# Optimization experiments

Measured on AMD Instinct MI355X. Metric: run time of the kernel, lower is better.

The kernel has to match this reference:

```python
import jax, jax.numpy as jnp
import numpy as np

D_MODEL = 4096
N_HEADS = 32
N_KV_HEADS = 8
HEAD_DIM = D_MODEL // N_HEADS  # 128
SEQ = 2048
BATCH = 1
ROPE_BASE = 10000.0


def build_rope_cache(max_seq_len, head_dim, base=10000.0):
    half = head_dim // 2
    pos = jnp.arange(max_seq_len, dtype=jnp.float32)
    inv_freqs = 1.0 / (base ** (jnp.arange(half, dtype=jnp.float32) / half))
    angles = pos[:, None] * inv_freqs[None, :]  # (S, half)
    return jnp.cos(angles), jnp.sin(angles)


def apply_rope(t, cos, sin):
    # t: (B, H, S, D); cos/sin: (S, D//2) broadcast over batch & heads.
    t_even = t[..., 0::2]
    t_odd = t[..., 1::2]
    c = cos[None, None, :, :]
    s = sin[None, None, :, :]
    rot_even = t_even * c - t_odd * s
    rot_odd = t_even * s + t_odd * c
    # interleave back into even/odd slots
    return jnp.stack([rot_even, rot_odd], axis=-1).reshape(t.shape)


def setup_inputs() -> dict:
    key = jax.random.key(0)
    kx, kq, kk, kv, ko = jax.random.split(key, 5)
    bound = 1.0 / np.sqrt(D_MODEL)
    x = jax.random.normal(kx, (BATCH, SEQ, D_MODEL), dtype=jnp.float32)
    # torch Linear weights: (out_features, in_features)
    wq = jax.random.uniform(kq, (N_HEADS * HEAD_DIM, D_MODEL), minval=-bound, maxval=bound, dtype=jnp.float32)
    wk = jax.random.uniform(kk, (N_KV_HEADS * HEAD_DIM, D_MODEL), minval=-bound, maxval=bound, dtype=jnp.float32)
    wv = jax.random.uniform(kv, (N_KV_HEADS * HEAD_DIM, D_MODEL), minval=-bound, maxval=bound, dtype=jnp.float32)
    wo = jax.random.uniform(ko, (D_MODEL, D_MODEL), minval=-bound, maxval=bound, dtype=jnp.float32)
    attn_mask = jnp.tril(jnp.ones((SEQ, SEQ), dtype=jnp.int32))[None, None, :, :]
    return {"x": x, "wq": wq, "wk": wk, "wv": wv, "wo": wo, "attn_mask": attn_mask}


def reference(x, wq, wk, wv, wo, attn_mask):
    B, S, _ = x.shape
    cos, sin = build_rope_cache(SEQ, HEAD_DIM, ROPE_BASE)
    cos, sin = cos[:S], sin[:S]
    q = (x @ wq.T).reshape(B, S, N_HEADS, HEAD_DIM).transpose(0, 2, 1, 3)      # (B,H,S,D)
    k = (x @ wk.T).reshape(B, S, N_KV_HEADS, HEAD_DIM).transpose(0, 2, 1, 3)   # (B,Hkv,S,D)
    v = (x @ wv.T).reshape(B, S, N_KV_HEADS, HEAD_DIM).transpose(0, 2, 1, 3)
    q = apply_rope(q, cos, sin)
    k = apply_rope(k, cos, sin)
    n_rep = N_HEADS // N_KV_HEADS
    if n_rep > 1:
        k = jnp.repeat(k, n_rep, axis=1)
        v = jnp.repeat(v, n_rep, axis=1)
    scores = jnp.einsum('bhqd,bhkd->bhqk', q, k) / jnp.sqrt(jnp.float32(HEAD_DIM))
    scores = jnp.where(attn_mask == 0, -jnp.inf, scores)
    attn = jax.nn.softmax(scores, axis=-1)
    out = jnp.einsum('bhqk,bhkd->bhqd', attn, v)
    out = out.transpose(0, 2, 1, 3).reshape(B, S, D_MODEL)
    return out @ wo.T
```

## Files before the change

### kernel.cpp

```cpp
#include <hip/hip_runtime.h>
#include <hip/hip_bf16.h>

typedef float f32x2 __attribute__((ext_vector_type(2)));
typedef float f32x4 __attribute__((ext_vector_type(4)));
typedef __bf16 bf16x4 __attribute__((ext_vector_type(4)));
typedef __bf16 bf16x8 __attribute__((ext_vector_type(8)));

__device__ __forceinline__ void gld_lds16(const void* g, void* l) {
  __builtin_amdgcn_global_load_lds((const __attribute__((address_space(1))) void*)g,
                                   (__attribute__((address_space(3))) void*)l, 16, 0, 0);
}

__global__ void cvt_f32_bf16(const float* __restrict__ in, __bf16* __restrict__ out,
                             int n8) {
  int idx = blockIdx.x * blockDim.x + threadIdx.x;
  if (idx >= n8) return;
  f32x4 a = *(const f32x4*)(in + (size_t)idx * 8);
  f32x4 b = *(const f32x4*)(in + (size_t)idx * 8 + 4);
  bf16x8 o;
#pragma unroll
  for (int j = 0; j < 4; ++j) { o[j] = (__bf16)a[j]; o[4 + j] = (__bf16)b[j]; }
  *(bf16x8*)(out + (size_t)idx * 8) = o;
}

__global__ void cvt_f32_bf16_2(const float* __restrict__ inA,
                               const float* __restrict__ inB,
                               __bf16* __restrict__ out, int n8half) {
  int idx = blockIdx.x * blockDim.x + threadIdx.x;
  if (idx >= 2 * n8half) return;
  const float* src = (idx < n8half) ? inA + (size_t)idx * 8
                                    : inB + (size_t)(idx - n8half) * 8;
  f32x4 a = *(const f32x4*)src;
  f32x4 b = *(const f32x4*)(src + 4);
  bf16x8 o;
#pragma unroll
  for (int j = 0; j < 4; ++j) { o[j] = (__bf16)a[j]; o[4 + j] = (__bf16)b[j]; }
  *(bf16x8*)(out + (size_t)idx * 8) = o;
}

__global__ void cvt_x_trig(const float* __restrict__ in, __bf16* __restrict__ out,
                           int n8, float* __restrict__ trig, int ntrig) {
  int idx = blockIdx.x * blockDim.x + threadIdx.x;
  if (idx < n8) {
    f32x4 a = *(const f32x4*)(in + (size_t)idx * 8);
    f32x4 b = *(const f32x4*)(in + (size_t)idx * 8 + 4);
    bf16x8 o;
#pragma unroll
    for (int j = 0; j < 4; ++j) { o[j] = (__bf16)a[j]; o[4 + j] = (__bf16)b[j]; }
    *(bf16x8*)(out + (size_t)idx * 8) = o;
  } else if (idx - n8 < ntrig) {
    int t = idx - n8;
    int i = t & 63, s = t >> 6;
    float ang = (float)s * powf(10000.0f, -(float)i * (1.0f / 64.0f));
    float sn, cs;
    sincosf(ang, &sn, &cs);
    trig[t * 2] = cs;
    trig[t * 2 + 1] = sn;
  }
}

template <int BM, int BN, typename OutT, bool KVF>
__global__ __launch_bounds__(256) void gemm_bf16(const __bf16* __restrict__ A,
                                                 const __bf16* __restrict__ B0,
                                                 const __bf16* __restrict__ B1,
                                                 int Nsplit, OutT* __restrict__ C,
                                                 int M, int N, int K,
                                                 const float* __restrict__ trig,
                                                 __bf16* __restrict__ Vt) {
  constexpr int MI = BM / 32, NJ = BN / 32;
  constexpr int RA = BM / 32, RB = BN / 32;
  __shared__ __bf16 As[BM * 64] __attribute__((aligned(16)));
  __shared__ __bf16 Bs[BN * 64] __attribute__((aligned(16)));

  const int tid = threadIdx.x;
  const int lane = tid & 63;
  const int w = tid >> 6;
  const int nwg = gridDim.x * gridDim.y;
  const int orig = blockIdx.y * gridDim.x + blockIdx.x;
  const int wgid = (orig & 7) * (nwg >> 3) + (orig >> 3);
  const int m0 = (wgid % gridDim.x) * BM;
  const int n0 = (wgid / gridDim.x) * BN;
  const int li = lane & 15, lg = lane >> 4;

  const __bf16* bsrc[RB];
#pragma unroll
  for (int i = 0; i < RB; ++i) {
    int slot = i * 256 + w * 64 + lane;
    int row = slot >> 3;
    int sch = (slot & 7) ^ (row & 7);
    int n = n0 + row;
    bsrc[i] = (n < Nsplit ? B0 + (size_t)n * K : B1 + (size_t)(n - Nsplit) * K) +
              sch * 8;
  }
  const __bf16* asrc[RA];
#pragma unroll
  for (int i = 0; i < RA; ++i) {
    int slot = i * 256 + w * 64 + lane;
    int row = slot >> 3;
    int sch = (slot & 7) ^ (row & 7);
    asrc[i] = A + (size_t)(m0 + row) * K + sch * 8;
  }

  const int wr = (w >> 1) * (BM / 2);
  const int wc = (w & 1) * (BN / 2);

  f32x4 acc[MI][NJ] = {};

  for (int k0 = 0; k0 < K; k0 += 64) {
    __syncthreads();
#pragma unroll
    for (int i = 0; i < RA; ++i)
      gld_lds16(asrc[i] + k0, &As[(i * 256 + w * 64) * 8]);
#pragma unroll
    for (int i = 0; i < RB; ++i)
      gld_lds16(bsrc[i] + k0, &Bs[(i * 256 + w * 64) * 8]);
    __syncthreads();

#pragma unroll
    for (int u = 0; u < 2; ++u) {
      bf16x8 af[MI], bfr[NJ];
#pragma unroll
      for (int mi = 0; mi < MI; ++mi)
        af[mi] = *(const bf16x8*)&As[(wr + mi * 16 + li) * 64 +
                                     (((u * 4 + lg) ^ (li & 7)) * 8)];
#pragma unroll
      for (int nj = 0; nj < NJ; ++nj)
        bfr[nj] = *(const bf16x8*)&Bs[(wc + nj * 16 + li) * 64 +
                                      (((u * 4 + lg) ^ (li & 7)) * 8)];
#pragma unroll
      for (int mi = 0; mi < MI; ++mi)
#pragma unroll
        for (int nj = 0; nj < NJ; ++nj)
          acc[mi][nj] = __builtin_amdgcn_mfma_f32_16x16x32_bf16(af[mi], bfr[nj],
                                                                acc[mi][nj], 0, 0, 0);
    }
  }

  const int crow = lg * 4;
  if (KVF && n0 >= Nsplit) {
#pragma unroll
    for (int mi = 0; mi < MI; ++mi)
#pragma unroll
      for (int nj = 0; nj < NJ; ++nj) {
        int d = n0 - Nsplit + wc + nj * 16 + li;
        int sb = m0 + wr + mi * 16 + crow;
        bf16x4 pk;
#pragma unroll
        for (int r = 0; r < 4; ++r) pk[r] = (__bf16)acc[mi][nj][r];
        *(bf16x4*)&Vt[(size_t)d * 2048 + sb] = pk;
      }
  } else if (KVF) {
#pragma unroll
    for (int mi = 0; mi < MI; ++mi)
#pragma unroll
      for (int nj = 0; nj < NJ; ++nj) {
        int c = n0 + wc + nj * 16 + li;
        int i = (c & 127) >> 1;
        bool even = (c & 1) == 0;
#pragma unroll
        for (int r = 0; r < 4; ++r) {
          int s = m0 + wr + mi * 16 + crow + r;
          float own = acc[mi][nj][r];
          float oth = __shfl_xor(own, 1);
          f32x2 cs = *(const f32x2*)&trig[((size_t)s * 64 + i) * 2];
          float v = even ? (own * cs[0] - oth * cs[1])
                         : (oth * cs[1] + own * cs[0]);
          C[(size_t)s * N + c] = (OutT)v;
        }
      }
  } else {
#pragma unroll
    for (int mi = 0; mi < MI; ++mi)
#pragma unroll
      for (int nj = 0; nj < NJ; ++nj)
#pragma unroll
        for (int r = 0; r < 4; ++r)
          C[(size_t)(m0 + wr + mi * 16 + crow + r) * N + (n0 + wc + nj * 16 + li)] =
              (OutT)acc[mi][nj][r];
  }
}

__global__ __launch_bounds__(256) void attn_fwd_v11(const __bf16* __restrict__ Q,
                                                    const __bf16* __restrict__ KVb,
                                                    const __bf16* __restrict__ Vt,
                                                    const float* __restrict__ trig,
                                                    __bf16* __restrict__ O,
                                                    const float* __restrict__ wo,
                                                    __bf16* __restrict__ wob) {
  const int tid = threadIdx.x;
  const int lane = tid & 63;
  const int w = tid >> 6;
  const int bid = blockIdx.x;
  const int xcd = bid & 7;
  const int r9 = bid >> 3;
  const int h = xcd * 4 + (r9 & 3);
  const int mb = 31 - (r9 >> 2);
  const int kvh = h >> 2;
  const int m0 = mb * 64;
  const int rbase = m0 + w * 16;

  __shared__ __bf16 Ks[3][32 * 128] __attribute__((aligned(16)));
  __shared__ __bf16 Vs[3][128 * 32] __attribute__((aligned(16)));
  __shared__ __bf16 Ps[4][16 * 40] __attribute__((aligned(16)));

  const int li = lane & 15, lg = lane >> 4;
  const float qscale = 0.08838834764831845f * 1.4426950408889634f;

  auto stage_k = [&](int k0, int buf) {
#pragma unroll
    for (int i = 0; i < 2; ++i) {
      int slot = i * 256 + tid;
      int row = slot >> 4;
      int sch = (slot & 15) ^ (row & 7);
      gld_lds16(&KVb[(size_t)(k0 + row) * 2048 + kvh * 128 + sch * 8],
                &Ks[buf][(i * 256 + w * 64) * 8]);
    }
  };
  auto stage_v = [&](int k0, int buf) {
#pragma unroll
    for (int i = 0; i < 2; ++i) {
      int slot = i * 256 + tid;
      int row = slot >> 2;
      int sch = (slot & 3) ^ ((row >> 1) & 3);
      gld_lds16(&Vt[(size_t)(kvh * 128 + row) * 2048 + k0 + sch * 8],
                &Vs[buf][(i * 256 + w * 64) * 8]);
    }
  };

  const int s = rbase + li;
  bf16x8 qf[4];
  {
    const __bf16* qrow = Q + (size_t)s * 4096 + h * 128;
#pragma unroll
    for (int kc = 0; kc < 4; ++kc) {
      bf16x8 raw = *(const bf16x8*)(qrow + kc * 32 + lg * 8);
#pragma unroll
      for (int jj = 0; jj < 4; ++jj) {
        int i = kc * 16 + lg * 4 + jj;
        f32x2 cs = *(const f32x2*)&trig[((size_t)s * 64 + i) * 2];
        float e = (float)raw[2 * jj], o = (float)raw[2 * jj + 1];
        qf[kc][2 * jj]     = (__bf16)((e * cs[0] - o * cs[1]) * qscale);
        qf[kc][2 * jj + 1] = (__bf16)((e * cs[1] + o * cs[0]) * qscale);
      }
    }
  }

  f32x4 accO[8] = {};
  float pl[4] = {0.f, 0.f, 0.f, 0.f};
  const int ntile = 2 * (mb + 1);

  stage_v(0, 0);
  stage_k(0, 0);

#pragma unroll 1
  for (int t = 0; t < ntile; ++t) {
    const int k0 = t * 32;
    const int cb = t % 3;
    const int nk = (t + 1 < ntile) ? k0 + 32 : k0;
    stage_v(nk, (t + 1) % 3);
    stage_k(nk, (t + 1) % 3);

    asm volatile("s_waitcnt vmcnt(4)" ::: "memory");
    __builtin_amdgcn_s_barrier();
    __builtin_amdgcn_sched_barrier(0);

    f32x4 s2[2] = {};
    __builtin_amdgcn_s_setprio(1);
#pragma unroll
    for (int nt = 0; nt < 2; ++nt)
#pragma unroll
      for (int kc = 0; kc < 4; ++kc) {
        bf16x8 kf = *(const bf16x8*)&Ks[cb][(li + 16 * nt) * 128 +
                                           (((4 * kc + lg) ^ (li & 7)) * 8)];
        s2[nt] = __builtin_amdgcn_mfma_f32_16x16x32_bf16(kf, qf[kc], s2[nt], 0, 0, 0);
      }
    __builtin_amdgcn_s_setprio(0);

    if (k0 + 31 > rbase) {
#pragma unroll
      for (int nt = 0; nt < 2; ++nt) {
        bf16x4 pk;
#pragma unroll
        for (int rr = 0; rr < 4; ++rr) {
          const int key = k0 + 16 * nt + lg * 4 + rr;
          float v = s2[nt][rr];
          if (key > s) v = -INFINITY;
          float p = exp2f(v);
          pl[rr] += p;
          pk[rr] = (__bf16)p;
        }
        *(bf16x4*)&Ps[w][li * 40 + 16 * nt + lg * 4] = pk;
      }
    } else {
#pragma unroll
      for (int nt = 0; nt < 2; ++nt) {
        bf16x4 pk;
#pragma unroll
        for (int rr = 0; rr < 4; ++rr) {
          float p = exp2f(s2[nt][rr]);
          pl[rr] += p;
          pk[rr] = (__bf16)p;
        }
        *(bf16x4*)&Ps[w][li * 40 + 16 * nt + lg * 4] = pk;
      }
    }
    bf16x8 pa = *(const bf16x8*)&Ps[w][li * 40 + lg * 8];

    __builtin_amdgcn_s_setprio(1);
#pragma unroll
    for (int dt = 0; dt < 8; ++dt) {
      bf16x8 vf = *(const bf16x8*)&Vs[cb][(li + 16 * dt) * 32 +
                                          ((lg ^ ((li >> 1) & 3)) * 8)];
      accO[dt] = __builtin_amdgcn_mfma_f32_16x16x32_bf16(pa, vf, accO[dt], 0, 0, 0);
    }
    __builtin_amdgcn_s_setprio(0);
  }

  {
    float sum = (pl[0] + pl[1]) + (pl[2] + pl[3]);
    sum += __shfl_xor(sum, 16);
    sum += __shfl_xor(sum, 32);
    float inv[4];
#pragma unroll
    for (int rr = 0; rr < 4; ++rr) inv[rr] = 1.0f / __shfl(sum, lg * 4 + rr);
#pragma unroll
    for (int dt = 0; dt < 8; ++dt)
#pragma unroll
      for (int rr = 0; rr < 4; ++rr)
        O[(size_t)(rbase + lg * 4 + rr) * 4096 + h * 128 + dt * 16 + li] =
            (__bf16)(accO[dt][rr] * inv[rr]);
  }

  if (mb <= 23) {
    const int u = (23 - mb) + 24 * ((r9 & 3) + 4 * xcd);
    const int n8 = 4096 * 4096 / 8;
    for (int idx = u * 256 + tid; idx < n8; idx += 768 * 256) {
      f32x4 a = *(const f32x4*)(wo + (size_t)idx * 8);
      f32x4 b = *(const f32x4*)(wo + (size_t)idx * 8 + 4);
      bf16x8 o;
#pragma unroll
      for (int j = 0; j < 4; ++j) { o[j] = (__bf16)a[j]; o[4 + j] = (__bf16)b[j]; }
      *(bf16x8*)(wob + (size_t)idx * 8) = o;
    }
  }
}

extern "C" void kernel_launch(void* const* d_in, const int* in_sizes, int n_in,
                              void* d_out, int out_size, void* d_ws, size_t ws_size,
                              hipStream_t stream) {
  const float* x  = (const float*)d_in[0];
  const float* wq = (const float*)d_in[1];
  const float* wk = (const float*)d_in[2];
  const float* wv = (const float*)d_in[3];
  const float* wo = (const float*)d_in[4];
  float* out = (float*)d_out;

  const int S = 2048, D = 4096;
  char* ws = (char*)d_ws;
  __bf16* xb  = (__bf16*)ws;
  __bf16* Qb  = (__bf16*)(ws + 16777216);
  __bf16* KVb = (__bf16*)(ws + 33554432);
  __bf16* Vt  = (__bf16*)(ws + 41943040);
  __bf16* wb  = (__bf16*)(ws + 46137344);
  float*  trig = (float*)(ws + 79691776);
  __bf16* AOb = xb;

  cvt_x_trig<<<(S * D / 8 + 2048 * 64 + 255) / 256, 256, 0, stream>>>(
      x, xb, S * D / 8, trig, 2048 * 64);

  cvt_f32_bf16<<<(D * D / 8 + 255) / 256, 256, 0, stream>>>(wq, wb, D * D / 8);
  gemm_bf16<128, 128, __bf16, false><<<dim3(16, 32), 256, 0, stream>>>(
      xb, wb, wb, 1 << 30, Qb, S, D, D, nullptr, nullptr);

  cvt_f32_bf16_2<<<(2 * 1024 * D / 8 + 255) / 256, 256, 0, stream>>>(
      wk, wv, wb, 1024 * D / 8);
  gemm_bf16<64, 128, __bf16, true><<<dim3(32, 16), 256, 0, stream>>>(
      xb, wb, wb + (size_t)1024 * D, 1024, KVb, S, 2048, D, trig, Vt);

  attn_fwd_v11<<<1024, 256, 0, stream>>>(Qb, KVb, Vt, trig, AOb, wo, wb);

  gemm_bf16<128, 128, float, false><<<dim3(16, 32), 256, 0, stream>>>(
      AOb, wb, wb, 1 << 30, out, S, D, D, nullptr, nullptr);
}
```

Measured before the change: 342.2 us.

## Fuse Q, K and V projections into one concatenated-weight GEMM launch

The separate Q GEMM (128x128 tiles) and K/V GEMM (64x128 tiles) are merged into one GEMM over a concatenated 6144-row bf16 weight. The epilogue routes each column tile by its N offset: to Q, to a RoPE-applied K buffer with 1024 stride, or to transposed V. This removes one launch and the tail of the smaller K/V GEMM, and gives the K/V part the larger tile and a 768-workgroup grid. K is now stored in its own compact buffer and the workspace is re-laid out, which needs more weight-buffer space.

```diff
diff --git a/kernel.cpp b/kernel.cpp
--- a/kernel.cpp
+++ b/kernel.cpp
@@ -59,18 +59,16 @@
   }
 }
 
-template <int BM, int BN, typename OutT, bool KVF>
+template <bool QKV3, typename OutT>
 __global__ __launch_bounds__(256) void gemm_bf16(const __bf16* __restrict__ A,
-                                                 const __bf16* __restrict__ B0,
-                                                 const __bf16* __restrict__ B1,
-                                                 int Nsplit, OutT* __restrict__ C,
-                                                 int M, int N, int K,
+                                                 const __bf16* __restrict__ B,
+                                                 OutT* __restrict__ C,
+                                                 __bf16* __restrict__ Kb,
+                                                 __bf16* __restrict__ Vt,
                                                  const float* __restrict__ trig,
-                                                 __bf16* __restrict__ Vt) {
-  constexpr int MI = BM / 32, NJ = BN / 32;
-  constexpr int RA = BM / 32, RB = BN / 32;
-  __shared__ __bf16 As[BM * 64] __attribute__((aligned(16)));
-  __shared__ __bf16 Bs[BN * 64] __attribute__((aligned(16)));
+                                                 int M, int N, int K) {
+  __shared__ __bf16 As[128 * 64] __attribute__((aligned(16)));
+  __shared__ __bf16 Bs[128 * 64] __attribute__((aligned(16)));
 
   const int tid = threadIdx.x;
   const int lane = tid & 63;
@@ -78,82 +76,80 @@
   const int nwg = gridDim.x * gridDim.y;
   const int orig = blockIdx.y * gridDim.x + blockIdx.x;
   const int wgid = (orig & 7) * (nwg >> 3) + (orig >> 3);
-  const int m0 = (wgid % gridDim.x) * BM;
-  const int n0 = (wgid / gridDim.x) * BN;
+  const int m0 = (wgid % gridDim.x) * 128;
+  const int n0 = (wgid / gridDim.x) * 128;
   const int li = lane & 15, lg = lane >> 4;
 
-  const __bf16* bsrc[RB];
-#pragma unroll
-  for (int i = 0; i < RB; ++i) {
+  const __bf16* bsrc[4];
+#pragma unroll
+  for (int i = 0; i < 4; ++i) {
     int slot = i * 256 + w * 64 + lane;
     int row = slot >> 3;
     int sch = (slot & 7) ^ (row & 7);
-    int n = n0 + row;
-    bsrc[i] = (n < Nsplit ? B0 + (size_t)n * K : B1 + (size_t)(n - Nsplit) * K) +
-              sch * 8;
-  }
-  const __bf16* asrc[RA];
-#pragma unroll
-  for (int i = 0; i < RA; ++i) {
+    bsrc[i] = B + (size_t)(n0 + row) * K + sch * 8;
+  }
+  const __bf16* asrc[4];
+#pragma unroll
+  for (int i = 0; i < 4; ++i) {
     int slot = i * 256 + w * 64 + lane;
     int row = slot >> 3;
     int sch = (slot & 7) ^ (row & 7);
     asrc[i] = A + (size_t)(m0 + row) * K + sch * 8;
   }
 
-  const int wr = (w >> 1) * (BM / 2);
-  const int wc = (w & 1) * (BN / 2);
-
-  f32x4 acc[MI][NJ] = {};
+  const int wr = (w >> 1) * 64;
+  const int wc = (w & 1) * 64;
+
+  f32x4 acc[4][4] = {};
 
   for (int k0 = 0; k0 < K; k0 += 64) {
     __syncthreads();
 #pragma unroll
-    for (int i = 0; i < RA; ++i)
+    for (int i = 0; i < 4; ++i)
       gld_lds16(asrc[i] + k0, &As[(i * 256 + w * 64) * 8]);
 #pragma unroll
-    for (int i = 0; i < RB; ++i)
+    for (int i = 0; i < 4; ++i)
       gld_lds16(bsrc[i] + k0, &Bs[(i * 256 + w * 64) * 8]);
     __syncthreads();
 
 #pragma unroll
     for (int u = 0; u < 2; ++u) {
-      bf16x8 af[MI], bfr[NJ];
-#pragma unroll
-      for (int mi = 0; mi < MI; ++mi)
+      bf16x8 af[4], bfr[4];
+#pragma unroll
+      for (int mi = 0; mi < 4; ++mi)
         af[mi] = *(const bf16x8*)&As[(wr + mi * 16 + li) * 64 +
                                      (((u * 4 + lg) ^ (li & 7)) * 8)];
 #pragma unroll
-      for (int nj = 0; nj < NJ; ++nj)
+      for (int nj = 0; nj < 4; ++nj)
         bfr[nj] = *(const bf16x8*)&Bs[(wc + nj * 16 + li) * 64 +
                                       (((u * 4 + lg) ^ (li & 7)) * 8)];
 #pragma unroll
-      for (int mi = 0; mi < MI; ++mi)
-#pragma unroll
-        for (int nj = 0; nj < NJ; ++nj)
+      for (int mi = 0; mi < 4; ++mi)
+#pragma unroll
+        for (int nj = 0; nj < 4; ++nj)
           acc[mi][nj] = __builtin_amdgcn_mfma_f32_16x16x32_bf16(af[mi], bfr[nj],
                                                                 acc[mi][nj], 0, 0, 0);
     }
   }
 
   const int crow = lg * 4;
-  if (KVF && n0 >= Nsplit) {
-#pragma unroll
-    for (int mi = 0; mi < MI; ++mi)
-#pragma unroll
-      for (int nj = 0; nj < NJ; ++nj) {
-        int d = n0 - Nsplit + wc + nj * 16 + li;
+  if (QKV3 && n0 >= 5120) {
+#pragma unroll
+    for (int mi = 0; mi < 4; ++mi)
+#pragma unroll
+      for (int nj = 0; nj < 4; ++nj) {
+        int d = n0 - 5120 + wc + nj * 16 + li;
         int sb = m0 + wr + mi * 16 + crow;
         bf16x4 pk;
 #pragma unroll
         for (int r = 0; r < 4; ++r) pk[r] = (__bf16)acc[mi][nj][r];
         *(bf16x4*)&Vt[(size_t)d * 2048 + sb] = pk;
       }
-  } else if (KVF) {
-#pragma unroll
-    for (int mi = 0; mi < MI; ++mi)
-#pragma unroll
-      for (int nj = 0; nj < NJ; ++nj) {
+  } else if (QKV3 && n0 >= 4096) {
+#pragma unroll
+    for (int mi = 0; mi < 4; ++mi)
+#pragma unroll
+      for (int nj = 0; nj < 4; ++nj) {
         int c = n0 + wc + nj * 16 + li;
         int i = (c & 127) >> 1;
         bool even = (c & 1) == 0;
@@ -165,23 +161,24 @@
           f32x2 cs = *(const f32x2*)&trig[((size_t)s * 64 + i) * 2];
           float v = even ? (own * cs[0] - oth * cs[1])
                          : (oth * cs[1] + own * cs[0]);
-          C[(size_t)s * N + c] = (OutT)v;
+          Kb[(size_t)s * 1024 + (c - 4096)] = (__bf16)v;
         }
       }
   } else {
-#pragma unroll
-    for (int mi = 0; mi < MI; ++mi)
-#pragma unroll
-      for (int nj = 0; nj < NJ; ++nj)
+    const int stride = QKV3 ? 4096 : N;
+#pragma unroll
+    for (int mi = 0; mi < 4; ++mi)
+#pragma unroll
+      for (int nj = 0; nj < 4; ++nj)
 #pragma unroll
         for (int r = 0; r < 4; ++r)
-          C[(size_t)(m0 + wr + mi * 16 + crow + r) * N + (n0 + wc + nj * 16 + li)] =
+          C[(size_t)(m0 + wr + mi * 16 + crow + r) * stride + (n0 + wc + nj * 16 + li)] =
               (OutT)acc[mi][nj][r];
   }
 }
 
 __global__ __launch_bounds__(256) void attn_fwd_v11(const __bf16* __restrict__ Q,
-                                                    const __bf16* __restrict__ KVb,
+                                                    const __bf16* __restrict__ Kb,
                                                     const __bf16* __restrict__ Vt,
                                                     const float* __restrict__ trig,
                                                     __bf16* __restrict__ O,
@@ -212,7 +209,7 @@
       int slot = i * 256 + tid;
       int row = slot >> 4;
       int sch = (slot & 15) ^ (row & 7);
-      gld_lds16(&KVb[(size_t)(k0 + row) * 2048 + kvh * 128 + sch * 8],
+      gld_lds16(&Kb[(size_t)(k0 + row) * 1024 + kvh * 128 + sch * 8],
                 &Ks[buf][(i * 256 + w * 64) * 8]);
     }
   };
@@ -359,26 +356,24 @@
   char* ws = (char*)d_ws;
   __bf16* xb  = (__bf16*)ws;
   __bf16* Qb  = (__bf16*)(ws + 16777216);
-  __bf16* KVb = (__bf16*)(ws + 33554432);
-  __bf16* Vt  = (__bf16*)(ws + 41943040);
-  __bf16* wb  = (__bf16*)(ws + 46137344);
-  float*  trig = (float*)(ws + 79691776);
+  __bf16* Kb  = (__bf16*)(ws + 33554432);
+  __bf16* Vt  = (__bf16*)(ws + 37748736);
+  __bf16* wb  = (__bf16*)(ws + 41943040);
+  float*  trig = (float*)(ws + 92274688);
   __bf16* AOb = xb;
 
   cvt_x_trig<<<(S * D / 8 + 2048 * 64 + 255) / 256, 256, 0, stream>>>(
       x, xb, S * D / 8, trig, 2048 * 64);
 
   cvt_f32_bf16<<<(D * D / 8 + 255) / 256, 256, 0, stream>>>(wq, wb, D * D / 8);
-  gemm_bf16<128, 128, __bf16, false><<<dim3(16, 32), 256, 0, stream>>>(
-      xb, wb, wb, 1 << 30, Qb, S, D, D, nullptr, nullptr);
-
   cvt_f32_bf16_2<<<(2 * 1024 * D / 8 + 255) / 256, 256, 0, stream>>>(
-      wk, wv, wb, 1024 * D / 8);
-  gemm_bf16<64, 128, __bf16, true><<<dim3(32, 16), 256, 0, stream>>>(
-      xb, wb, wb + (size_t)1024 * D, 1024, KVb, S, 2048, D, trig, Vt);
-
-  attn_fwd_v11<<<1024, 256, 0, stream>>>(Qb, KVb, Vt, trig, AOb, wo, wb);
-
-  gemm_bf16<128, 128, float, false><<<dim3(16, 32), 256, 0, stream>>>(
-      AOb, wb, wb, 1 << 30, out, S, D, D, nullptr, nullptr);
-}
+      wk, wv, wb + (size_t)D * D, 1024 * D / 8);
+
+  gemm_bf16<true, __bf16><<<dim3(16, 48), 256, 0, stream>>>(
+      xb, wb, Qb, Kb, Vt, trig, S, 6144, D);
+
+  attn_fwd_v11<<<1024, 256, 0, stream>>>(Qb, Kb, Vt, trig, AOb, wo, wb);
+
+  gemm_bf16<false, float><<<dim3(16, 32), 256, 0, stream>>>(
+      AOb, wb, out, nullptr, nullptr, nullptr, S, D, D);
+}
```

After: 353.1 us. 3.2% more time.
